# Kernel tuning notes

Measured on AMD Instinct MI355X. Metric: run time of the kernel, lower is better.

## Reference

```python
import jax, jax.numpy as jnp
import numpy as np


def setup_inputs() -> dict:
    key = jax.random.key(0)
    k1, k2, k3 = jax.random.split(key, 3)
    B, N, D = 512, 12, 4
    return {
        "x": jax.random.normal(k1, (B, N), dtype=jnp.float32),
        "rys": jax.random.normal(k2, (D, N), dtype=jnp.float32),
        "cnot_params": jax.random.normal(k3, (D, N - 1), dtype=jnp.float32),
    }


def _rx(state, theta, q, B):
    # RX(theta) = [[c, -i s], [-i s, c]], half-angle; theta: (B,)
    s = state.reshape(B, 2 ** q, 2, -1)
    c = jnp.cos(theta * 0.5)[:, None, None].astype(state.dtype)
    sn = (-1j * jnp.sin(theta * 0.5))[:, None, None].astype(state.dtype)
    a0, a1 = s[:, :, 0], s[:, :, 1]
    return jnp.stack([c * a0 + sn * a1, sn * a0 + c * a1], axis=2).reshape(B, -1)


def _ry(state, theta, q, B):
    # RY(theta) = [[c, -s], [s, c]], half-angle; theta: scalar (shared over batch)
    s = state.reshape(B, 2 ** q, 2, -1)
    c = jnp.cos(theta * 0.5).astype(state.dtype)
    sn = jnp.sin(theta * 0.5).astype(state.dtype)
    a0, a1 = s[:, :, 0], s[:, :, 1]
    return jnp.stack([c * a0 - sn * a1, sn * a0 + c * a1], axis=2).reshape(B, -1)


def _cnot(state, q, B):
    # CNOT on adjacent wires (control=q, target=q+1): flip target where control=1
    s = state.reshape(B, 2 ** q, 2, 2, -1)
    return jnp.stack([s[:, :, 0], s[:, :, 1, ::-1]], axis=2).reshape(B, -1)


def reference(x, rys, cnot_params):
    B, n = x.shape
    depth = rys.shape[0]
    # wire 0 is the most-significant bit (PennyLane convention)
    state = jnp.zeros((B, 2 ** n), dtype=jnp.complex64).at[:, 0].set(1.0)
    for q in range(n):
        state = _rx(state, x[:, q], q, B)
    for d in range(depth):
        for q in range(n):
            state = _ry(state, rys[d, q], q, B)
        for q in range(n - 1):  # cnot_params are declared but unused (CNOT is non-parametric)
            state = _cnot(state, q, B)
    probs = jnp.abs(state) ** 2  # (B, 2^n), real
    zs = []
    for q in range(n):
        p = probs.reshape(B, 2 ** q, 2, -1).sum(axis=(1, 3))  # (B, 2)
        zs.append(p[:, 0] - p[:, 1])
    return jnp.stack(zs, axis=1).astype(jnp.float32)  # (B, n)
```

## Files before the change

kernel.cpp:

```cpp
#include <hip/hip_runtime.h>

#define NQ 12
#define DIM 4096
#define BLK 256

typedef float v2f __attribute__((ext_vector_type(2)));

__host__ __device__ constexpr int igrayc(int v) {
    v ^= v >> 1; v ^= v >> 2; v ^= v >> 4; v ^= v >> 8;
    return v & (DIM - 1);
}
__host__ __device__ constexpr int gkf(int v, int k) {
    if (k == 1) v ^= v >> 1;
    else if (k == 2) v ^= v >> 2;
    else { v ^= v >> 2; v ^= v >> 1; }
    return v;
}
__host__ __device__ constexpr int sigf(int v) { return v ^ ((v >> 4) & 15); }
__host__ __device__ constexpr int TkF(int v, int k) { return sigf(gkf(v, k)); }

__device__ __forceinline__ v2f cmul(v2f a, v2f b) {
    v2f r; r.x = a.x * b.x - a.y * b.y; r.y = a.x * b.y + a.y * b.x; return r;
}
__device__ __forceinline__ void gate_pair(v2f& a0, v2f& a1, v2f cc, v2f ss, v2f ns) {
    v2f t0 = a0, t1 = a1;
    a0 = __builtin_elementwise_fma(ns, t1, cc * t0);
    a1 = __builtin_elementwise_fma(ss, t0, cc * t1);
}
template<int PB>
__device__ __forceinline__ void gate16(v2f (&a)[16], float c, float s) {
    const v2f cc = {c, c}, ss = {s, s}, ns = {-s, -s};
    #pragma unroll
    for (int j0 = 0; j0 < 16; ++j0) {
        if (j0 & PB) continue;
        gate_pair(a[j0], a[j0 | PB], cc, ss, ns);
    }
}
template<int K, int OSH>
__device__ __forceinline__ void ld16(const char* bufc, int sb8, v2f (&a)[16]) {
    #pragma unroll
    for (int j = 0; j < 16; ++j)
        a[j] = *(const v2f*)(bufc + (sb8 ^ (TkF(j << OSH, K) << 3)));
}
template<int K, int OSH>
__device__ __forceinline__ void st16(char* bufc, int sb8, const v2f (&a)[16]) {
    #pragma unroll
    for (int j = 0; j < 16; ++j)
        *(v2f*)(bufc + (sb8 ^ (TkF(j << OSH, K) << 3))) = a[j];
}

__device__ __forceinline__ float wave64_sum(float v) {
    v += __int_as_float(__builtin_amdgcn_update_dpp(0, __float_as_int(v), 0x111, 0xf, 0xf, true));
    v += __int_as_float(__builtin_amdgcn_update_dpp(0, __float_as_int(v), 0x112, 0xf, 0xf, true));
    v += __int_as_float(__builtin_amdgcn_update_dpp(0, __float_as_int(v), 0x114, 0xf, 0xf, true));
    v += __int_as_float(__builtin_amdgcn_update_dpp(0, __float_as_int(v), 0x118, 0xf, 0xf, true));
    v += __int_as_float(__builtin_amdgcn_update_dpp(0, __float_as_int(v), 0x142, 0xa, 0xf, false));
    v += __int_as_float(__builtin_amdgcn_update_dpp(0, __float_as_int(v), 0x143, 0xc, 0xf, false));
    return v;
}

__global__ __launch_bounds__(BLK, 2)
void qsim_kernel(const float* __restrict__ x,
                 const float* __restrict__ rys,
                 float* __restrict__ out) {
    __shared__ __align__(16) v2f buf[DIM];
    __shared__ float cr[4 * NQ], sr[4 * NQ];
    __shared__ v2f fac[NQ][2];
    __shared__ float zred[4][NQ];

    const int b = blockIdx.x;
    const int t = threadIdx.x;
    char* bufc = (char*)buf;

    if (t < 4 * NQ) {
        float th = 0.5f * rys[t];
        cr[t] = cosf(th); sr[t] = sinf(th);
    }
    if (t >= 64 && t < 64 + NQ) {
        int q = t - 64;
        float xh = 0.5f * x[b * NQ + q];
        float cx = cosf(xh), sx = sinf(xh);
        float th = 0.5f * rys[q];
        float c0 = cosf(th), s0 = sinf(th);
        int p = NQ - 1 - q;
        fac[p][0] = v2f{c0 * cx,  s0 * sx};
        fac[p][1] = v2f{s0 * cx, -c0 * sx};
    }
    __syncthreads();

    const int nbB  = (t & 15) | (((t >> 4) & 15) << 8);
    const int nbA4 = ((t & 3) << 4) | (((t >> 2) & 3) << 8)
                   | (((t >> 4) & 3) << 6) | (((t >> 6) & 3) << 10);
    const int nbA7 = ((t & 1) << 4) | (((t >> 1) & 7) << 8)
                   | (((t >> 4) & 3) << 5) | (((t >> 6) & 1) << 7)
                   | (((t >> 7) & 1) << 11);

    {
        v2f a[16];
        const int Mb = t ^ (t >> 1);
        v2f P = fac[0][Mb & 1];
        #pragma unroll
        for (int p = 1; p < 7; ++p) P = cmul(P, fac[p][(Mb >> p) & 1]);
        const int b7 = (Mb >> 7) & 1;
        v2f E = cmul(P, fac[7][b7]);
        v2f O = cmul(P, fac[7][b7 ^ 1]);
        v2f L4[4], H4[4];
        #pragma unroll
        for (int v = 0; v < 4; ++v) {
            L4[v] = cmul(fac[8][v & 1],  fac[9][(v >> 1) & 1]);
            H4[v] = cmul(fac[10][v & 1], fac[11][(v >> 1) & 1]);
        }
        #pragma unroll
        for (int j = 0; j < 16; ++j) {
            const int gv = (j ^ (j >> 1)) & 15;
            a[j] = cmul((j & 1) ? O : E, cmul(L4[gv & 3], H4[(gv >> 2) & 3]));
        }
        gate16<1>(a, cr[15], sr[15]);
        gate16<2>(a, cr[14], sr[14]);
        gate16<4>(a, cr[13], sr[13]);
        gate16<8>(a, cr[12], sr[12]);
        st16<1, 8>(bufc, TkF(t, 1) << 3, a);
    }
    __syncthreads();

    #define GATE_PASS(K, NB, OSH, I0, I1, I2, I3)                 \
    {                                                             \
        const int sb8 = TkF(NB, K) << 3;                          \
        v2f a[16];                                                \
        ld16<K, OSH>(bufc, sb8, a);                               \
        gate16<1>(a, cr[I0], sr[I0]);                             \
        gate16<2>(a, cr[I1], sr[I1]);                             \
        gate16<4>(a, cr[I2], sr[I2]);                             \
        gate16<8>(a, cr[I3], sr[I3]);                             \
        st16<K, OSH>(bufc, sb8, a);                               \
    }                                                             \
    __syncthreads();

    GATE_PASS(1, (t << 4), 0, 23, 22, 21, 20)
    GATE_PASS(1, nbB,      4, 19, 18, 17, 16)
    GATE_PASS(2, t,        8, 27, 26, 25, 24)
    GATE_PASS(2, nbA4,     0, 35, 34, 33, 32)
    GATE_PASS(2, nbB,      4, 31, 30, 29, 28)
    GATE_PASS(3, t,        8, 39, 38, 37, 36)
    GATE_PASS(3, nbA7,     0, 47, 46, 45, 44)
    #undef GATE_PASS

    {
        const int sb8 = TkF(nbB, 3) << 3;
        v2f a[16];
        ld16<3, 4>(bufc, sb8, a);
        gate16<1>(a, cr[43], sr[43]);
        gate16<2>(a, cr[42], sr[42]);
        gate16<4>(a, cr[41], sr[41]);
        gate16<8>(a, cr[40], sr[40]);

        float pr[16];
        #pragma unroll
        for (int j = 0; j < 16; ++j)
            pr[j] = a[j].x * a[j].x + a[j].y * a[j].y;
        #pragma unroll
        for (int bit = 1; bit < 16; bit <<= 1) {
            #pragma unroll
            for (int j = 0; j < 16; ++j) {
                if (j & bit) continue;
                float u = pr[j], w = pr[j | bit];
                pr[j] = u + w;
                pr[j | bit] = u - w;
            }
        }
        const int R = igrayc(nbB);
        #pragma unroll
        for (int q = 0; q < NQ; ++q) {
            const int l = NQ - 1 - q;
            const float cf = (l <= 4) ? pr[15]
                           : (l == 5) ? pr[14]
                           : (l == 6) ? pr[12]
                           : (l == 7) ? pr[8]  : pr[0];
            float v = ((R >> l) & 1) ? -cf : cf;
            v = wave64_sum(v);
            if ((t & 63) == 63) zred[t >> 6][q] = v;
        }
    }
    __syncthreads();
    if (t < NQ)
        out[b * NQ + t] = zred[0][t] + zred[1][t] + zred[2][t] + zred[3][t];
}

extern "C" void kernel_launch(void* const* d_in, const int* in_sizes, int n_in,
                              void* d_out, int out_size, void* d_ws, size_t ws_size,
                              hipStream_t stream) {
    const float* x   = (const float*)d_in[0];
    const float* rys = (const float*)d_in[1];
    float* out = (float*)d_out;
    qsim_kernel<<<512, BLK, 0, stream>>>(x, rys, out);
}
```

Measured before the change: 17.20 us.

## Apply low-qubit gates via DPP lane shuffles to cut shared-memory passes

Replaces several LDS load/gate/store passes with register-level gates that exchange amplitudes between lanes through DPP permutes (xor 1, 2, 7, 15 patterns). A new per-thread index mapping is introduced so four qubits live across lanes, merging two passes into one and cutting barriers and LDS traffic from seven passes to four. In exchange it adds many DPP moves per gate, and it depends on the lane mapping and the sign choice being correct.

```diff
diff --git a/kernel.cpp b/kernel.cpp
--- a/kernel.cpp
+++ b/kernel.cpp
@@ -36,6 +36,24 @@
         gate_pair(a[j0], a[j0 | PB], cc, ss, ns);
     }
 }
+
+template<int CTRL, int BETA>
+__device__ __forceinline__ void dpp_gate16(v2f (&a)[16], float c, float s, int lb) {
+    const float sl = ((lb >> BETA) & 1) ? s : -s;
+    const v2f cc = {c, c}, sv = {sl, sl};
+    #pragma unroll
+    for (int j = 0; j < 16; ++j) {
+        int bx = __builtin_amdgcn_update_dpp(0, __float_as_int(a[j].x), CTRL, 0xf, 0xf, true);
+        int by = __builtin_amdgcn_update_dpp(0, __float_as_int(a[j].y), CTRL, 0xf, 0xf, true);
+        v2f b; b.x = __int_as_float(bx); b.y = __int_as_float(by);
+        a[j] = __builtin_elementwise_fma(sv, b, cc * a[j]);
+    }
+}
+#define DPP_XOR1  0xB1
+#define DPP_XOR2  0x4E
+#define DPP_XOR7  0x141
+#define DPP_XOR15 0x140
+
 template<int K, int OSH>
 __device__ __forceinline__ void ld16(const char* bufc, int sb8, v2f (&a)[16]) {
     #pragma unroll
@@ -88,12 +106,8 @@
     }
     __syncthreads();
 
-    const int nbB  = (t & 15) | (((t >> 4) & 15) << 8);
-    const int nbA4 = ((t & 3) << 4) | (((t >> 2) & 3) << 8)
-                   | (((t >> 4) & 3) << 6) | (((t >> 6) & 3) << 10);
-    const int nbA7 = ((t & 1) << 4) | (((t >> 1) & 7) << 8)
-                   | (((t >> 4) & 3) << 5) | (((t >> 6) & 1) << 7)
-                   | (((t >> 7) & 1) << 11);
+    const int lb = (t & 3) ^ (((t >> 2) & 1) * 7) ^ (((t >> 3) & 1) * 12)
+                 ^ ((t >> 4) << 8);
 
     {
         v2f a[16];
@@ -123,36 +137,55 @@
     }
     __syncthreads();
 
-    #define GATE_PASS(K, NB, OSH, I0, I1, I2, I3)                 \
-    {                                                             \
-        const int sb8 = TkF(NB, K) << 3;                          \
-        v2f a[16];                                                \
-        ld16<K, OSH>(bufc, sb8, a);                               \
-        gate16<1>(a, cr[I0], sr[I0]);                             \
-        gate16<2>(a, cr[I1], sr[I1]);                             \
-        gate16<4>(a, cr[I2], sr[I2]);                             \
-        gate16<8>(a, cr[I3], sr[I3]);                             \
-        st16<K, OSH>(bufc, sb8, a);                               \
-    }                                                             \
-    __syncthreads();
-
-    GATE_PASS(1, (t << 4), 0, 23, 22, 21, 20)
-    GATE_PASS(1, nbB,      4, 19, 18, 17, 16)
-    GATE_PASS(2, t,        8, 27, 26, 25, 24)
-    GATE_PASS(2, nbA4,     0, 35, 34, 33, 32)
-    GATE_PASS(2, nbB,      4, 31, 30, 29, 28)
-    GATE_PASS(3, t,        8, 39, 38, 37, 36)
-    GATE_PASS(3, nbA7,     0, 47, 46, 45, 44)
-    #undef GATE_PASS
+    #define AB_PASS(K, D)                                          \
+    {                                                              \
+        const int sb8 = TkF(lb, K) << 3;                           \
+        v2f a[16];                                                 \
+        ld16<K, 4>(bufc, sb8, a);                                  \
+        gate16<1>(a, cr[(D)*NQ + 7], sr[(D)*NQ + 7]);              \
+        gate16<2>(a, cr[(D)*NQ + 6], sr[(D)*NQ + 6]);              \
+        gate16<4>(a, cr[(D)*NQ + 5], sr[(D)*NQ + 5]);              \
+        gate16<8>(a, cr[(D)*NQ + 4], sr[(D)*NQ + 4]);              \
+        dpp_gate16<DPP_XOR1,  0>(a, cr[(D)*NQ + 11], sr[(D)*NQ + 11], lb); \
+        dpp_gate16<DPP_XOR2,  1>(a, cr[(D)*NQ + 10], sr[(D)*NQ + 10], lb); \
+        dpp_gate16<DPP_XOR7,  2>(a, cr[(D)*NQ + 9],  sr[(D)*NQ + 9],  lb); \
+        dpp_gate16<DPP_XOR15, 3>(a, cr[(D)*NQ + 8],  sr[(D)*NQ + 8],  lb); \
+        st16<K, 4>(bufc, sb8, a);                                  \
+    }                                                              \
+    __syncthreads();
+
+    #define C_PASS(K, I0, I1, I2, I3)                              \
+    {                                                              \
+        const int sb8 = TkF(t, K) << 3;                            \
+        v2f a[16];                                                 \
+        ld16<K, 8>(bufc, sb8, a);                                  \
+        gate16<1>(a, cr[I0], sr[I0]);                              \
+        gate16<2>(a, cr[I1], sr[I1]);                              \
+        gate16<4>(a, cr[I2], sr[I2]);                              \
+        gate16<8>(a, cr[I3], sr[I3]);                              \
+        st16<K, 8>(bufc, sb8, a);                                  \
+    }                                                              \
+    __syncthreads();
+
+    AB_PASS(1, 1)
+    C_PASS(2, 27, 26, 25, 24)
+    AB_PASS(2, 2)
+    C_PASS(3, 39, 38, 37, 36)
+    #undef AB_PASS
+    #undef C_PASS
 
     {
-        const int sb8 = TkF(nbB, 3) << 3;
+        const int sb8 = TkF(lb, 3) << 3;
         v2f a[16];
         ld16<3, 4>(bufc, sb8, a);
         gate16<1>(a, cr[43], sr[43]);
         gate16<2>(a, cr[42], sr[42]);
         gate16<4>(a, cr[41], sr[41]);
         gate16<8>(a, cr[40], sr[40]);
+        dpp_gate16<DPP_XOR1,  0>(a, cr[47], sr[47], lb);
+        dpp_gate16<DPP_XOR2,  1>(a, cr[46], sr[46], lb);
+        dpp_gate16<DPP_XOR7,  2>(a, cr[45], sr[45], lb);
+        dpp_gate16<DPP_XOR15, 3>(a, cr[44], sr[44], lb);
 
         float pr[16];
         #pragma unroll
@@ -168,7 +201,7 @@
                 pr[j | bit] = u - w;
             }
         }
-        const int R = igrayc(nbB);
+        const int R = igrayc(lb);
         #pragma unroll
         for (int q = 0; q < NQ; ++q) {
             const int l = NQ - 1 - q;
```

Measured after the change: 16.74 us. -2.7%, faster.
